# Kernel optimization log

Hardware: AMD Instinct MI355X
Metric: run time of the kernel (lower is better)

## Reference

```python
import jax, jax.numpy as jnp
import numpy as np

B, N, K, D = 2, 4096, 20, 128
PH = 8          # pos_mlp hidden dim
AH = 4 * D      # attn_mlp hidden dim (attn_mlp_hidden_mult=4)


def setup_inputs() -> dict:
    key = jax.random.key(0)
    ks = jax.random.split(key, 12)
    s = 0.02
    f32 = jnp.float32
    return {
        "x": jax.random.normal(ks[0], (B, N, 3), f32),
        "pos": jax.random.normal(ks[1], (B, N, 3), f32),
        # linear1/2/3 (torch Linear: y = x @ W.T + b)
        "W1": jax.random.normal(ks[2], (D, 3), f32) * s,  "b1": jnp.zeros((D,), f32),
        "W2": jax.random.normal(ks[3], (D, D), f32) * s,  "b2": jnp.zeros((D,), f32),
        "W3": jax.random.normal(ks[4], (D, D), f32) * s,  "b3": jnp.zeros((D,), f32),
        # PointTransformerLayer params
        "Wqkv": jax.random.normal(ks[5], (3 * D, D), f32) * s,          # to_qkv, no bias
        "Wp1": jax.random.normal(ks[6], (PH, 3), f32) * s,  "bp1": jnp.zeros((PH,), f32),
        "Wp2": jax.random.normal(ks[7], (D, PH), f32) * s,  "bp2": jnp.zeros((D,), f32),
        "Wa1": jax.random.normal(ks[8], (AH, D), f32) * s,  "ba1": jnp.zeros((AH,), f32),
        "Wa2": jax.random.normal(ks[9], (D, AH), f32) * s,  "ba2": jnp.zeros((D,), f32),
    }


def reference(x, pos, W1, b1, W2, b2, W3, b3, Wqkv,
              Wp1, bp1, Wp2, bp2, Wa1, ba1, Wa2, ba2):
    h = x @ W1.T + b1            # [B,N,D] linear1
    h1 = h @ W2.T + b2           # [B,N,D] linear2

    # --- PointTransformerLayer (lucidrains, KNN vector attention) ---
    qkv = h1 @ Wqkv.T            # [B,N,3D]
    q, k, v = jnp.split(qkv, 3, axis=-1)

    # squared pairwise distances and K nearest neighbors (self included)
    d2 = jnp.sum((pos[:, :, None, :] - pos[:, None, :, :]) ** 2, axis=-1)  # [B,N,N]
    _, idx = jax.lax.top_k(-d2, K)                                          # [B,N,K]

    gather = jax.vmap(lambda arr, ind: arr[ind])  # per-batch gather -> [B,N,K,*]
    kn = gather(k, idx)          # [B,N,K,D]
    vn = gather(v, idx)          # [B,N,K,D]
    pn = gather(pos, idx)        # [B,N,K,3]

    rel = pos[:, :, None, :] - pn                                   # [B,N,K,3]
    pe = jax.nn.relu(rel @ Wp1.T + bp1) @ Wp2.T + bp2               # pos_mlp [B,N,K,D]

    vn = vn + pe
    sim = jax.nn.relu((q[:, :, None, :] - kn + pe) @ Wa1.T + ba1) @ Wa2.T + ba2  # attn_mlp
    attn = jax.nn.softmax(sim, axis=2)                              # softmax over neighbors
    agg = jnp.sum(attn * vn, axis=2)                                # [B,N,D]

    return h + (agg @ W3.T + b3)  # residual: x + linear3(x1)
```

## Files before the change

### kernel.cpp

```cpp
#include <hip/hip_runtime.h>
#include <stdint.h>

#define BB 2
#define NN 4096
#define KNB 20
#define DD 128
#define PHH 8
#define AHH 512
#define BN (BB*NN)

typedef unsigned short ushort_t;
typedef short bf16x8 __attribute__((ext_vector_type(8)));
typedef float f32x4 __attribute__((ext_vector_type(4)));

__device__ __forceinline__ uint32_t umin32(uint32_t a, uint32_t b) { return a < b ? a : b; }
__device__ __forceinline__ uint32_t umax32(uint32_t a, uint32_t b) { return a > b ? a : b; }

__device__ __forceinline__ float bf2f(ushort_t u) {
    union { float f; uint32_t i; } c; c.i = ((uint32_t)u) << 16; return c.f;
}
__device__ __forceinline__ uint32_t cvt_pk_bf16(float lo, float hi) {
    uint32_t r;
    asm("v_cvt_pk_bf16_f32 %0, %1, %2" : "=v"(r) : "v"(lo), "v"(hi));
    return r;
}
__device__ __forceinline__ ushort_t f2bf(float f) {
    return (ushort_t)(cvt_pk_bf16(f, f) & 0xFFFFu);
}
__device__ __forceinline__ bf16x8 load_bfrag(const float* __restrict__ src) {
    float4 x = *(const float4*)src;
    float4 y = *(const float4*)(src + 4);
    union { bf16x8 v; uint32_t u[4]; } r;
    r.u[0] = cvt_pk_bf16(x.x, x.y);
    r.u[1] = cvt_pk_bf16(x.z, x.w);
    r.u[2] = cvt_pk_bf16(y.x, y.y);
    r.u[3] = cvt_pk_bf16(y.z, y.w);
    return r.v;
}

#define SW256(m, byteInRow) ((m)*256 + ((byteInRow) ^ (((m)&7) << 4)))

__global__ __launch_bounds__(256) void k_prep(
        const float* __restrict__ Wa1f, const float* __restrict__ Wa2f,
        const float* __restrict__ W3f, const float* __restrict__ W2f,
        const float* __restrict__ Wqkvf, const float* __restrict__ Wp2f,
        const float* __restrict__ pos,
        ushort_t* __restrict__ Wa1bf, ushort_t* __restrict__ Wa2bf,
        ushort_t* __restrict__ W3bf, ushort_t* __restrict__ W2bf,
        ushort_t* __restrict__ Wqkvbf, ushort_t* __restrict__ Wfusebf,
        float* __restrict__ psoa) {
    int bid = blockIdx.x, tid = threadIdx.x;
    if (bid < 64) {
        int base = bid * 2048 + tid * 8;
        const float* src = (base < 65536) ? (Wa1f + base) : (Wa2f + (base - 65536));
        ushort_t* dst = (base < 65536) ? (Wa1bf + base) : (Wa2bf + (base - 65536));
        union { ushort_t u[8]; uint4 q; } pk;
        #pragma unroll
        for (int i = 0; i < 8; ++i) pk.u[i] = f2bf(src[i]);
        *(uint4*)dst = pk.q;
    } else if (bid < 72) {
        int base = (bid - 64) * 2048 + tid * 8;
        union { ushort_t u[8]; uint4 q; } pk;
        #pragma unroll
        for (int i = 0; i < 8; ++i) pk.u[i] = f2bf(W3f[base + i]);
        *(uint4*)&W3bf[base] = pk.q;
    } else if (bid < 80) {
        int base = (bid - 72) * 2048 + tid * 8;
        union { ushort_t u[8]; uint4 q; } pk;
        #pragma unroll
        for (int i = 0; i < 8; ++i) pk.u[i] = f2bf(W2f[base + i]);
        *(uint4*)&W2bf[base] = pk.q;
    } else if (bid < 104) {
        int base = (bid - 80) * 2048 + tid * 8;
        union { ushort_t u[8]; uint4 q; } pk;
        #pragma unroll
        for (int i = 0; i < 8; ++i) pk.u[i] = f2bf(Wqkvf[base + i]);
        *(uint4*)&Wqkvbf[base] = pk.q;
    } else if (bid < 106) {
        int a = (bid - 104) * 256 + tid;
        float s[PHH];
        #pragma unroll
        for (int jj = 0; jj < PHH; ++jj) s[jj] = 0.f;
        for (int d = 0; d < DD; ++d) {
            float wv = Wa1f[(size_t)a*DD + d];
            #pragma unroll
            for (int jj = 0; jj < PHH; ++jj) s[jj] += wv * Wp2f[d*PHH + jj];
        }
        union { ushort_t u[8]; uint4 q; } pk;
        #pragma unroll
        for (int jj = 0; jj < PHH; ++jj) pk.u[jj] = f2bf(s[jj]);
        *(uint4*)&Wfusebf[a*PHH] = pk.q;
    } else {
        int e0 = (bid - 106) * 2048 + tid * 8;
        float v[8];
        #pragma unroll
        for (int i = 0; i < 8; ++i) {
            int el = e0 + i;
            int comp = el >> 13;
            int rem = el & 8191;
            v[i] = pos[(size_t)rem*3 + comp];
        }
        #pragma unroll
        for (int i = 0; i < 8; i += 4)
            *(float4*)&psoa[e0 + i] = (float4){v[i], v[i+1], v[i+2], v[i+3]};
    }
}

__global__ __launch_bounds__(256) void k_front(
        const float* __restrict__ x,
        const float* __restrict__ W1, const float* __restrict__ b1,
        const ushort_t* __restrict__ W2bf, const float* __restrict__ b2,
        const ushort_t* __restrict__ Wqkvbf,
        const ushort_t* __restrict__ Wa1bf, const float* __restrict__ ba1,
        float* __restrict__ h, ushort_t* __restrict__ vf,
        ushort_t* __restrict__ QWbf, ushort_t* __restrict__ KWbf) {
    __shared__ __align__(16) char smem[16896];
    float* xs = (float*)(smem + 16384);
    int tid = threadIdx.x, w = tid >> 6, lane = tid & 63;
    int lg = lane >> 4, c16 = lane & 15;
    int p0 = blockIdx.x * 32;

    if (tid < 96) xs[tid] = x[(size_t)p0*3 + tid];
    __syncthreads();

    #pragma unroll
    for (int it = 0; it < 16; ++it) {
        int lin = it*256 + tid;
        int m = lin >> 7, d = lin & 127;
        float hv = b1[d] + xs[m*3+0]*W1[d*3+0] + xs[m*3+1]*W1[d*3+1] + xs[m*3+2]*W1[d*3+2];
        h[(size_t)(p0+m)*DD + d] = hv;
        *(ushort_t*)&smem[SW256(m, d*2)] = f2bf(hv);
    }
    __syncthreads();

    {
        f32x4 acc[2][2];
        #pragma unroll
        for (int mt = 0; mt < 2; ++mt)
            #pragma unroll
            for (int ntl = 0; ntl < 2; ++ntl) acc[mt][ntl] = (f32x4){0,0,0,0};
        #pragma unroll
        for (int ks = 0; ks < 4; ++ks) {
            int k0 = ks*32 + lg*8;
            bf16x8 aF[2];
            #pragma unroll
            for (int mt = 0; mt < 2; ++mt)
                aF[mt] = *(const bf16x8*)&smem[SW256(mt*16 + c16, k0*2)];
            #pragma unroll
            for (int ntl = 0; ntl < 2; ++ntl) {
                int n = (2*w + ntl)*16 + c16;
                bf16x8 bF = *(const bf16x8*)&W2bf[(size_t)n*DD + k0];
                #pragma unroll
                for (int mt = 0; mt < 2; ++mt)
                    acc[mt][ntl] = __builtin_amdgcn_mfma_f32_16x16x32_bf16(aF[mt], bF, acc[mt][ntl], 0, 0, 0);
            }
        }
        #pragma unroll
        for (int ntl = 0; ntl < 2; ++ntl) {
            int n = (2*w + ntl)*16 + c16;
            float bias = b2[n];
            #pragma unroll
            for (int mt = 0; mt < 2; ++mt)
                #pragma unroll
                for (int i = 0; i < 4; ++i) {
                    int m = mt*16 + lg*4 + i;
                    *(ushort_t*)&smem[8192 + SW256(m, n*2)] = f2bf(acc[mt][ntl][i] + bias);
                }
        }
    }
    __syncthreads();

    {
        f32x4 acc[2][6];
        #pragma unroll
        for (int mt = 0; mt < 2; ++mt)
            #pragma unroll
            for (int ntl = 0; ntl < 6; ++ntl) acc[mt][ntl] = (f32x4){0,0,0,0};
        #pragma unroll
        for (int ks = 0; ks < 4; ++ks) {
            int k0 = ks*32 + lg*8;
            bf16x8 aF[2];
            #pragma unroll
            for (int mt = 0; mt < 2; ++mt)
                aF[mt] = *(const bf16x8*)&smem[8192 + SW256(mt*16 + c16, k0*2)];
            #pragma unroll
            for (int ntl = 0; ntl < 6; ++ntl) {
                int n = (w*6 + ntl)*16 + c16;
                bf16x8 bF = *(const bf16x8*)&Wqkvbf[(size_t)n*DD + k0];
                #pragma unroll
                for (int mt = 0; mt < 2; ++mt)
                    acc[mt][ntl] = __builtin_amdgcn_mfma_f32_16x16x32_bf16(aF[mt], bF, acc[mt][ntl], 0, 0, 0);
            }
        }
        #pragma unroll
        for (int ntl = 0; ntl < 6; ++ntl) {
            int n = (w*6 + ntl)*16 + c16;
            int r = n >> 7, d = n & 127;
            #pragma unroll
            for (int mt = 0; mt < 2; ++mt)
                #pragma unroll
                for (int i = 0; i < 4; ++i) {
                    int m = mt*16 + lg*4 + i;
                    if (r == 0) *(ushort_t*)&smem[SW256(m, d*2)] = f2bf(acc[mt][ntl][i]);
                    else if (r == 2) vf[(size_t)(p0+m)*DD + d] = f2bf(acc[mt][ntl][i]);
                }
        }
        __syncthreads();
        #pragma unroll
        for (int ntl = 0; ntl < 6; ++ntl) {
            int n = (w*6 + ntl)*16 + c16;
            int r = n >> 7, d = n & 127;
            if (r == 1) {
                #pragma unroll
                for (int mt = 0; mt < 2; ++mt)
                    #pragma unroll
                    for (int i = 0; i < 4; ++i) {
                        int m = mt*16 + lg*4 + i;
                        *(ushort_t*)&smem[8192 + SW256(m, d*2)] = f2bf(acc[mt][ntl][i]);
                    }
            }
        }
    }
    __syncthreads();

    #pragma unroll
    for (int half = 0; half < 2; ++half) {
        f32x4 accQ[2][4], accK[2][4];
        #pragma unroll
        for (int mt = 0; mt < 2; ++mt)
            #pragma unroll
            for (int ntl = 0; ntl < 4; ++ntl) {
                accQ[mt][ntl] = (f32x4){0,0,0,0};
                accK[mt][ntl] = (f32x4){0,0,0,0};
            }
        #pragma unroll
        for (int ks = 0; ks < 4; ++ks) {
            int k0 = ks*32 + lg*8;
            bf16x8 aQ[2], aK[2];
            #pragma unroll
            for (int mt = 0; mt < 2; ++mt) {
                aQ[mt] = *(const bf16x8*)&smem[SW256(mt*16 + c16, k0*2)];
                aK[mt] = *(const bf16x8*)&smem[8192 + SW256(mt*16 + c16, k0*2)];
            }
            #pragma unroll
            for (int ntl = 0; ntl < 4; ++ntl) {
                int n = (w*8 + half*4 + ntl)*16 + c16;
                bf16x8 bF = *(const bf16x8*)&Wa1bf[(size_t)n*DD + k0];
                #pragma unroll
                for (int mt = 0; mt < 2; ++mt) {
                    accQ[mt][ntl] = __builtin_amdgcn_mfma_f32_16x16x32_bf16(aQ[mt], bF, accQ[mt][ntl], 0, 0, 0);
                    accK[mt][ntl] = __builtin_amdgcn_mfma_f32_16x16x32_bf16(aK[mt], bF, accK[mt][ntl], 0, 0, 0);
                }
            }
        }
        #pragma unroll
        for (int ntl = 0; ntl < 4; ++ntl) {
            int n = (w*8 + half*4 + ntl)*16 + c16;
            float bias = ba1[n];
            #pragma unroll
            for (int mt = 0; mt < 2; ++mt)
                #pragma unroll
                for (int i = 0; i < 4; ++i) {
                    int m = mt*16 + lg*4 + i;
                    QWbf[(size_t)(p0+m)*AHH + n] = f2bf(accQ[mt][ntl][i] + bias);
                    KWbf[(size_t)(p0+m)*AHH + n] = f2bf(accK[mt][ntl][i]);
                }
        }
    }
}

__global__ __launch_bounds__(256) void k_knn(const float* __restrict__ pos,
                                             const float* __restrict__ psoa,
                                             int* __restrict__ idx) {
    int wid  = threadIdx.x >> 6;
    int lane = threadIdx.x & 63;
    int p = blockIdx.x*4 + wid;
    int b = p >> 12;
    float qx = pos[p*3+0], qy = pos[p*3+1], qz = pos[p*3+2];
    const float4* px4 = (const float4*)(psoa + (size_t)b*NN);
    const float4* py4 = (const float4*)(psoa + 8192 + (size_t)b*NN);
    const float4* pz4 = (const float4*)(psoa + 16384 + (size_t)b*NN);

    uint32_t bk[KNB];
    #pragma unroll
    for (int i = 0; i < KNB; ++i) bk[i] = 0xFFFFFFFFu;

    for (int it = 0; it < NN/256; ++it) {
        int j4 = it*64 + lane;
        float4 X = px4[j4], Y = py4[j4], Z = pz4[j4];
        #pragma unroll
        for (int c = 0; c < 4; ++c) {
            float dx = qx - ((c==0)?X.x:(c==1)?X.y:(c==2)?X.z:X.w);
            float dy = qy - ((c==0)?Y.x:(c==1)?Y.y:(c==2)?Y.z:Y.w);
            float dz = qz - ((c==0)?Z.x:(c==1)?Z.y:(c==2)?Z.z:Z.w);
            float d2 = dx*dx + dy*dy + dz*dz;
            uint32_t key = (__float_as_uint(d2) & 0xFFFFF000u) | (uint32_t)(j4*4 + c);
            if (key < bk[KNB-1]) {
                uint32_t cc = key;
                #pragma unroll
                for (int t = 0; t < KNB; ++t) {
                    uint32_t lo = umin32(cc, bk[t]);
                    uint32_t hi = umax32(cc, bk[t]);
                    bk[t] = lo; cc = hi;
                }
            }
        }
    }
    for (int r = 0; r < KNB; ++r) {
        uint32_t m = bk[0];
        #pragma unroll
        for (int s = 1; s < 64; s <<= 1)
            m = umin32(m, (uint32_t)__shfl_xor((int)m, s, 64));
        if (lane == 0) idx[(size_t)p*KNB + r] = (int)(m & 0xFFFu);
        bool win = (bk[0] == m);
        #pragma unroll
        for (int t = 0; t < KNB-1; ++t) bk[t] = win ? bk[t+1] : bk[t];
        bk[KNB-1] = win ? 0xFFFFFFFFu : bk[KNB-1];
    }
}

#define TL_OFF 0
#define PH_OFF 20480
#define NIDX_OFF 21760

__global__ __launch_bounds__(256, 4) void k_attn(
        const float* __restrict__ pos,
        const ushort_t* __restrict__ QWbf, const ushort_t* __restrict__ KWbf,
        const ushort_t* __restrict__ vf, const int* __restrict__ idx,
        const float* __restrict__ Wp1, const float* __restrict__ bp1,
        const float* __restrict__ Wp2, const float* __restrict__ bp2,
        const ushort_t* __restrict__ Wfusebf,
        const ushort_t* __restrict__ Wa2bf, const float* __restrict__ ba2,
        const ushort_t* __restrict__ W3bf, const float* __restrict__ b3,
        const float* __restrict__ h, float* __restrict__ out) {
    __shared__ __align__(16) char smem[22080];
    int* nidx = (int*)(smem + NIDX_OFF);

    int tid = threadIdx.x, w = tid >> 6, lane = tid & 63;
    int lg = lane >> 4, c16 = lane & 15;
    int bid = blockIdx.x;
    int xcd = bid & 7, sloc = bid >> 3;
    int b = xcd >> 2;
    int p0 = b*NN + ((xcd & 3)*256 + sloc)*4;

    if (tid < 80) nidx[tid] = idx[(size_t)(p0 + tid/20)*KNB + (tid%20)];
    __syncthreads();

    if (tid < 80) {
        int m = tid, g = m / 20;
        int j = nidx[m];
        const float* pq = pos + (size_t)(p0+g)*3;
        const float* pn = pos + (size_t)(b*NN+j)*3;
        float r0 = pq[0]-pn[0], r1 = pq[1]-pn[1], r2 = pq[2]-pn[2];
        union { ushort_t u[8]; uint4 q; } pk;
        #pragma unroll
        for (int jj = 0; jj < PHH; ++jj) {
            float a = bp1[jj] + r0*Wp1[jj*3+0] + r1*Wp1[jj*3+1] + r2*Wp1[jj*3+2];
            pk.u[jj] = f2bf(fmaxf(a, 0.f));
        }
        *(uint4*)&smem[PH_OFF + m*16] = pk.q;
    }
    __syncthreads();

    int dA = w*32 + 2*c16, dB = dA + 1;
    float bp2A = bp2[dA], bp2B = bp2[dB];
    float ba2A = ba2[dA], ba2B = ba2[dB];

    bf16x8 bP0 = {0,0,0,0,0,0,0,0}, bP1 = {0,0,0,0,0,0,0,0};
    if (lg == 0) {
        bP0 = load_bfrag(Wp2 + (size_t)dA*PHH);
        bP1 = load_bfrag(Wp2 + (size_t)dB*PHH);
    }
    uint32_t vpe_pk[5][4];
    #pragma unroll
    for (int mt = 0; mt < 5; ++mt) {
        bf16x8 aP = {0,0,0,0,0,0,0,0};
        if (lg == 0) aP = *(const bf16x8*)&smem[PH_OFF + (mt*16 + c16)*16];
        f32x4 accP0 = (f32x4){0,0,0,0}, accP1 = (f32x4){0,0,0,0};
        accP0 = __builtin_amdgcn_mfma_f32_16x16x32_bf16(aP, bP0, accP0, 0, 0, 0);
        accP1 = __builtin_amdgcn_mfma_f32_16x16x32_bf16(aP, bP1, accP1, 0, 0, 0);
        #pragma unroll
        for (int i = 0; i < 4; ++i) {
            int m = mt*16 + lg*4 + i;
            int j = nidx[m];
            uint32_t vw = *(const uint32_t*)&vf[(size_t)(b*NN+j)*DD + dA];
            float peA = accP0[i] + bp2A;
            float peB = accP1[i] + bp2B;
            vpe_pk[mt][i] = cvt_pk_bf16(bf2f((ushort_t)(vw & 0xFFFFu)) + peA,
                                        bf2f((ushort_t)(vw >> 16)) + peB);
        }
    }

    f32x4 accS[5][2];
    #pragma unroll
    for (int mt = 0; mt < 5; ++mt)
        #pragma unroll
        for (int ntl = 0; ntl < 2; ++ntl) accS[mt][ntl] = (f32x4){0,0,0,0};

    for (int c = 0; c < 4; ++c) {
        int aQ0 = c*128 + dA;
        bf16x8 bF0 = {0,0,0,0,0,0,0,0}, bF1 = {0,0,0,0,0,0,0,0};
        if (lg == 0) {
            bF0 = *(const bf16x8*)&Wfusebf[(size_t)aQ0*PHH];
            bF1 = *(const bf16x8*)&Wfusebf[(size_t)(aQ0+1)*PHH];
        }
        uint32_t qww[4];
        #pragma unroll
        for (int g = 0; g < 4; ++g)
            qww[g] = *(const uint32_t*)&QWbf[(size_t)(p0+g)*AHH + aQ0];
        uint32_t kwn[4];
        #pragma unroll
        for (int i = 0; i < 4; ++i)
            kwn[i] = *(const uint32_t*)&KWbf[(size_t)(b*NN + nidx[lg*4 + i])*AHH + aQ0];
        #pragma unroll
        for (int mt = 0; mt < 5; ++mt) {
            uint32_t kwc[4];
            #pragma unroll
            for (int i = 0; i < 4; ++i) kwc[i] = kwn[i];
            if (mt < 4) {
                #pragma unroll
                for (int i = 0; i < 4; ++i)
                    kwn[i] = *(const uint32_t*)&KWbf[(size_t)(b*NN + nidx[(mt+1)*16 + lg*4 + i])*AHH + aQ0];
            }
            bf16x8 aP = {0,0,0,0,0,0,0,0};
            if (lg == 0) aP = *(const bf16x8*)&smem[PH_OFF + (mt*16 + c16)*16];
            f32x4 accF0 = (f32x4){0,0,0,0}, accF1 = (f32x4){0,0,0,0};
            accF0 = __builtin_amdgcn_mfma_f32_16x16x32_bf16(aP, bF0, accF0, 0, 0, 0);
            accF1 = __builtin_amdgcn_mfma_f32_16x16x32_bf16(aP, bF1, accF1, 0, 0, 0);
            uint32_t qsel = (mt==0) ? qww[0]
                          : (mt==1) ? (lg>=1 ? qww[1] : qww[0])
                          : (mt==2) ? (lg>=2 ? qww[2] : qww[1])
                          : (mt==3) ? (lg==3 ? qww[3] : qww[2])
                          : qww[3];
            float qA = bf2f((ushort_t)(qsel & 0xFFFFu));
            float qB = bf2f((ushort_t)(qsel >> 16));
            #pragma unroll
            for (int i = 0; i < 4; ++i) {
                int m = mt*16 + lg*4 + i;
                float kA = bf2f((ushort_t)(kwc[i] & 0xFFFFu));
                float kB = bf2f((ushort_t)(kwc[i] >> 16));
                float tA = fmaxf(qA - kA + accF0[i], 0.f);
                float tB = fmaxf(qB - kB + accF1[i], 0.f);
                *(uint32_t*)&smem[TL_OFF + SW256(m, dA*2)] = cvt_pk_bf16(tA, tB);
            }
        }
        __syncthreads();

        __builtin_amdgcn_s_setprio(1);
        #pragma unroll
        for (int ks = 0; ks < 4; ++ks) {
            int k0 = ks*32 + lg*8;
            bf16x8 aF[5];
            #pragma unroll
            for (int mt = 0; mt < 5; ++mt)
                aF[mt] = *(const bf16x8*)&smem[TL_OFF + SW256(mt*16 + c16, k0*2)];
            bf16x8 bW0 = *(const bf16x8*)&Wa2bf[(size_t)dA*AHH + c*128 + k0];
            bf16x8 bW1 = *(const bf16x8*)&Wa2bf[(size_t)dB*AHH + c*128 + k0];
            #pragma unroll
            for (int mt = 0; mt < 5; ++mt) {
                accS[mt][0] = __builtin_amdgcn_mfma_f32_16x16x32_bf16(aF[mt], bW0, accS[mt][0], 0, 0, 0);
                accS[mt][1] = __builtin_amdgcn_mfma_f32_16x16x32_bf16(aF[mt], bW1, accS[mt][1], 0, 0, 0);
            }
        }
        __builtin_amdgcn_s_setprio(0);
        __syncthreads();
    }

    float s_mtA[5], a_mtA[5], s_mtB[5], a_mtB[5];
    #pragma unroll
    for (int mt = 0; mt < 5; ++mt) {
        float sa = 0.f, aa = 0.f, sb = 0.f, ab = 0.f;
        #pragma unroll
        for (int i = 0; i < 4; ++i) {
            float eA = __expf(accS[mt][0][i] + ba2A);
            float eB = __expf(accS[mt][1][i] + ba2B);
            uint32_t pk = vpe_pk[mt][i];
            float vA = bf2f((ushort_t)(pk & 0xFFFFu));
            float vB = bf2f((ushort_t)(pk >> 16));
            sa += eA; aa += eA*vA;
            sb += eB; ab += eB*vB;
        }
        s_mtA[mt] = sa; a_mtA[mt] = aa; s_mtB[mt] = sb; a_mtB[mt] = ab;
    }
    bool eq0 = (lg==0), ge1 = (lg>=1), ge2 = (lg>=2), le1 = (lg<=1), le2 = (lg<=2), eq3 = (lg==3);
    float s0A = s_mtA[0] + (eq0 ? s_mtA[1] : 0.f);
    float s1A = (ge1 ? s_mtA[1] : 0.f) + (le1 ? s_mtA[2] : 0.f);
    float s2A = (ge2 ? s_mtA[2] : 0.f) + (le2 ? s_mtA[3] : 0.f);
    float s3A = (eq3 ? s_mtA[3] : 0.f) + s_mtA[4];
    float a0A = a_mtA[0] + (eq0 ? a_mtA[1] : 0.f);
    float a1A = (ge1 ? a_mtA[1] : 0.f) + (le1 ? a_mtA[2] : 0.f);
    float a2A = (ge2 ? a_mtA[2] : 0.f) + (le2 ? a_mtA[3] : 0.f);
    float a3A = (eq3 ? a_mtA[3] : 0.f) + a_mtA[4];
    float s0B = s_mtB[0] + (eq0 ? s_mtB[1] : 0.f);
    float s1B = (ge1 ? s_mtB[1] : 0.f) + (le1 ? s_mtB[2] : 0.f);
    float s2B = (ge2 ? s_mtB[2] : 0.f) + (le2 ? s_mtB[3] : 0.f);
    float s3B = (eq3 ? s_mtB[3] : 0.f) + s_mtB[4];
    float a0B = a_mtB[0] + (eq0 ? a_mtB[1] : 0.f);
    float a1B = (ge1 ? a_mtB[1] : 0.f) + (le1 ? a_mtB[2] : 0.f);
    float a2B = (ge2 ? a_mtB[2] : 0.f) + (le2 ? a_mtB[3] : 0.f);
    float a3B = (eq3 ? a_mtB[3] : 0.f) + a_mtB[4];

    #define RED2(v) { v += __shfl_xor(v, 16, 64); v += __shfl_xor(v, 32, 64); }
    RED2(s0A) RED2(s1A) RED2(s2A) RED2(s3A)
    RED2(a0A) RED2(a1A) RED2(a2A) RED2(a3A)
    RED2(s0B) RED2(s1B) RED2(s2B) RED2(s3B)
    RED2(a0B) RED2(a1B) RED2(a2B) RED2(a3B)
    #undef RED2

    float myS_A = (lg==0) ? s0A : (lg==1) ? s1A : (lg==2) ? s2A : s3A;
    float myA_A = (lg==0) ? a0A : (lg==1) ? a1A : (lg==2) ? a2A : a3A;
    float myS_B = (lg==0) ? s0B : (lg==1) ? s1B : (lg==2) ? s2B : s3B;
    float myA_B = (lg==0) ? a0B : (lg==1) ? a1B : (lg==2) ? a2B : a3B;
    float aggA = myA_A / myS_A;
    float aggB = myA_B / myS_B;

    float hv[2][4];
    if (lg == 0) {
        #pragma unroll
        for (int ntl = 0; ntl < 2; ++ntl) {
            int n = (w*2 + ntl)*16 + c16;
            #pragma unroll
            for (int i = 0; i < 4; ++i)
                hv[ntl][i] = h[(size_t)(p0+i)*DD + n];
        }
    }
    #pragma unroll
    for (int z = 0; z < 3; ++z)
        *(uint32_t*)&smem[TL_OFF + 1024 + (z*256 + tid)*4] = 0u;
    *(uint32_t*)&smem[TL_OFF + SW256(lg, dA*2)] = cvt_pk_bf16(aggA, aggB);
    __syncthreads();

    f32x4 accO[2];
    accO[0] = (f32x4){0,0,0,0}; accO[1] = (f32x4){0,0,0,0};
    #pragma unroll
    for (int ks = 0; ks < 4; ++ks) {
        int k0 = ks*32 + lg*8;
        bf16x8 aF = *(const bf16x8*)&smem[TL_OFF + SW256(c16, k0*2)];
        #pragma unroll
        for (int ntl = 0; ntl < 2; ++ntl) {
            int n = (w*2 + ntl)*16 + c16;
            bf16x8 bF = *(const bf16x8*)&W3bf[(size_t)n*DD + k0];
            accO[ntl] = __builtin_amdgcn_mfma_f32_16x16x32_bf16(aF, bF, accO[ntl], 0, 0, 0);
        }
    }
    if (lg == 0) {
        #pragma unroll
        for (int ntl = 0; ntl < 2; ++ntl) {
            int n = (w*2 + ntl)*16 + c16;
            float bias = b3[n];
            #pragma unroll
            for (int i = 0; i < 4; ++i) {
                size_t o = (size_t)(p0+i)*DD + n;
                out[o] = accO[ntl][i] + bias + hv[ntl][i];
            }
        }
    }
}

extern "C" void kernel_launch(void* const* d_in, const int* in_sizes, int n_in,
                              void* d_out, int out_size, void* d_ws, size_t ws_size,
                              hipStream_t stream) {
    const float* x    = (const float*)d_in[0];
    const float* pos  = (const float*)d_in[1];
    const float* W1   = (const float*)d_in[2];
    const float* b1   = (const float*)d_in[3];
    const float* W2   = (const float*)d_in[4];
    const float* b2   = (const float*)d_in[5];
    const float* W3   = (const float*)d_in[6];
    const float* b3   = (const float*)d_in[7];
    const float* Wqkv = (const float*)d_in[8];
    const float* Wp1  = (const float*)d_in[9];
    const float* bp1  = (const float*)d_in[10];
    const float* Wp2  = (const float*)d_in[11];
    const float* bp2  = (const float*)d_in[12];
    const float* Wa1  = (const float*)d_in[13];
    const float* ba1  = (const float*)d_in[14];
    const float* Wa2  = (const float*)d_in[15];
    const float* ba2  = (const float*)d_in[16];

    char* W = (char*)d_ws;
    float*    h       = (float*)(W + 0);
    ushort_t* vf      = (ushort_t*)(W + 8388608);
    ushort_t* QWbf    = (ushort_t*)(W + 10485760);
    ushort_t* KWbf    = (ushort_t*)(W + 18874368);
    int*      idx     = (int*)(W + 27262976);
    ushort_t* Wa1bf   = (ushort_t*)(W + 27918336);
    ushort_t* Wa2bf   = (ushort_t*)(W + 28049408);
    ushort_t* Wfusebf = (ushort_t*)(W + 28180480);
    float*    psoa    = (float*)(W + 28188672);
    ushort_t* W3bf    = (ushort_t*)(W + 28286976);
    ushort_t* W2bf    = (ushort_t*)(W + 28319744);
    ushort_t* Wqkvbf  = (ushort_t*)(W + 28352512);

    k_prep <<<118, 256, 0, stream>>>(Wa1, Wa2, W3, W2, Wqkv, Wp2, pos,
                                     Wa1bf, Wa2bf, W3bf, W2bf, Wqkvbf, Wfusebf, psoa);
    k_front<<<BN/32, 256, 0, stream>>>(x, W1, b1, W2bf, b2, Wqkvbf, Wa1bf, ba1,
                                       h, vf, QWbf, KWbf);
    k_knn  <<<BN/4, 256, 0, stream>>>(pos, psoa, idx);
    k_attn <<<BN/4, 256, 0, stream>>>(pos, QWbf, KWbf, vf, idx,
                                      Wp1, bp1, Wp2, bp2, Wfusebf, Wa2bf, ba2,
                                      W3bf, b3, h, (float*)d_out);
}
```

Before: 159.0 us.

## Order attention query points by Morton cell to improve neighbor-gather locality

Adds two extra blocks to the front kernel that bucket each batch's points into a 16^3 Morton-coded grid, using a counting sort with shared-memory atomics, and write a permutation. The attention kernel then processes query points in this spatially sorted order, so blocks that run near each other gather overlapping KNN neighbor rows of KW and v, which is meant to raise L2/cache hit rates. The cost is an extra indirection per query and scattered writes to the output, and the order within a cell is nondeterministic because of the atomics.

```diff
diff --git a/kernel.cpp b/kernel.cpp
--- a/kernel.cpp
+++ b/kernel.cpp
@@ -36,6 +36,15 @@
     r.u[2] = cvt_pk_bf16(y.x, y.y);
     r.u[3] = cvt_pk_bf16(y.z, y.w);
     return r.v;
+}
+__device__ __forceinline__ uint32_t exp3b(uint32_t v) {
+    return (v & 1u) | ((v & 2u) << 2) | ((v & 4u) << 4) | ((v & 8u) << 6);
+}
+__device__ __forceinline__ uint32_t mcell(float x, float y, float z) {
+    uint32_t ux = (uint32_t)fminf(fmaxf((x + 4.f) * 2.f, 0.f), 15.f);
+    uint32_t uy = (uint32_t)fminf(fmaxf((y + 4.f) * 2.f, 0.f), 15.f);
+    uint32_t uz = (uint32_t)fminf(fmaxf((z + 4.f) * 2.f, 0.f), 15.f);
+    return (exp3b(ux) << 2) | (exp3b(uy) << 1) | exp3b(uz);
 }
 
 #define SW256(m, byteInRow) ((m)*256 + ((byteInRow) ^ (((m)&7) << 4)))
@@ -107,18 +116,57 @@
 }
 
 __global__ __launch_bounds__(256) void k_front(
-        const float* __restrict__ x,
+        const float* __restrict__ x, const float* __restrict__ posg,
         const float* __restrict__ W1, const float* __restrict__ b1,
         const ushort_t* __restrict__ W2bf, const float* __restrict__ b2,
         const ushort_t* __restrict__ Wqkvbf,
         const ushort_t* __restrict__ Wa1bf, const float* __restrict__ ba1,
         float* __restrict__ h, ushort_t* __restrict__ vf,
-        ushort_t* __restrict__ QWbf, ushort_t* __restrict__ KWbf) {
-    __shared__ __align__(16) char smem[16896];
+        ushort_t* __restrict__ QWbf, ushort_t* __restrict__ KWbf,
+        int* __restrict__ perm) {
+    __shared__ __align__(16) char smem[17408];
+    int tid = threadIdx.x, bid = blockIdx.x;
+
+    if (bid >= BN/32) {
+        int bb = bid - BN/32;
+        uint32_t* cnt  = (uint32_t*)smem;
+        uint32_t* part = (uint32_t*)(smem + 16384);
+        const float* pb = posg + (size_t)bb*NN*3;
+        for (int i = tid; i < 4096; i += 256) cnt[i] = 0;
+        __syncthreads();
+        for (int i = tid; i < NN; i += 256) {
+            uint32_t c = mcell(pb[i*3+0], pb[i*3+1], pb[i*3+2]);
+            atomicAdd(&cnt[c], 1u);
+        }
+        __syncthreads();
+        uint32_t s = 0;
+        #pragma unroll
+        for (int j = 0; j < 16; ++j) s += cnt[tid*16 + j];
+        part[tid] = s;
+        __syncthreads();
+        if (tid == 0) {
+            uint32_t run = 0;
+            for (int i = 0; i < 256; ++i) { uint32_t c = part[i]; part[i] = run; run += c; }
+        }
+        __syncthreads();
+        {
+            uint32_t run = part[tid];
+            #pragma unroll
+            for (int j = 0; j < 16; ++j) { uint32_t c = cnt[tid*16 + j]; cnt[tid*16 + j] = run; run += c; }
+        }
+        __syncthreads();
+        for (int i = tid; i < NN; i += 256) {
+            uint32_t c = mcell(pb[i*3+0], pb[i*3+1], pb[i*3+2]);
+            uint32_t posn = atomicAdd(&cnt[c], 1u);
+            perm[(size_t)bb*NN + posn] = bb*NN + i;
+        }
+        return;
+    }
+
     float* xs = (float*)(smem + 16384);
-    int tid = threadIdx.x, w = tid >> 6, lane = tid & 63;
+    int w = tid >> 6, lane = tid & 63;
     int lg = lane >> 4, c16 = lane & 15;
-    int p0 = blockIdx.x * 32;
+    int p0 = bid * 32;
 
     if (tid < 96) xs[tid] = x[(size_t)p0*3 + tid];
     __syncthreads();
@@ -322,34 +370,39 @@
 #define TL_OFF 0
 #define PH_OFF 20480
 #define NIDX_OFF 21760
+#define QP_OFF 22080
 
 __global__ __launch_bounds__(256, 4) void k_attn(
         const float* __restrict__ pos,
         const ushort_t* __restrict__ QWbf, const ushort_t* __restrict__ KWbf,
         const ushort_t* __restrict__ vf, const int* __restrict__ idx,
+        const int* __restrict__ perm,
         const float* __restrict__ Wp1, const float* __restrict__ bp1,
         const float* __restrict__ Wp2, const float* __restrict__ bp2,
         const ushort_t* __restrict__ Wfusebf,
         const ushort_t* __restrict__ Wa2bf, const float* __restrict__ ba2,
         const ushort_t* __restrict__ W3bf, const float* __restrict__ b3,
         const float* __restrict__ h, float* __restrict__ out) {
-    __shared__ __align__(16) char smem[22080];
+    __shared__ __align__(16) char smem[22096];
     int* nidx = (int*)(smem + NIDX_OFF);
+    int* qpS  = (int*)(smem + QP_OFF);
 
     int tid = threadIdx.x, w = tid >> 6, lane = tid & 63;
     int lg = lane >> 4, c16 = lane & 15;
     int bid = blockIdx.x;
     int xcd = bid & 7, sloc = bid >> 3;
     int b = xcd >> 2;
-    int p0 = b*NN + ((xcd & 3)*256 + sloc)*4;
-
-    if (tid < 80) nidx[tid] = idx[(size_t)(p0 + tid/20)*KNB + (tid%20)];
+    int slot4 = ((xcd & 3)*256 + sloc)*4;
+
+    if (tid < 4) qpS[tid] = perm[(size_t)b*NN + slot4 + tid];
+    __syncthreads();
+    if (tid < 80) nidx[tid] = idx[(size_t)qpS[tid/20]*KNB + (tid%20)];
     __syncthreads();
 
     if (tid < 80) {
         int m = tid, g = m / 20;
         int j = nidx[m];
-        const float* pq = pos + (size_t)(p0+g)*3;
+        const float* pq = pos + (size_t)qpS[g]*3;
         const float* pn = pos + (size_t)(b*NN+j)*3;
         float r0 = pq[0]-pn[0], r1 = pq[1]-pn[1], r2 = pq[2]-pn[2];
         union { ushort_t u[8]; uint4 q; } pk;
@@ -407,7 +460,7 @@
         uint32_t qww[4];
         #pragma unroll
         for (int g = 0; g < 4; ++g)
-            qww[g] = *(const uint32_t*)&QWbf[(size_t)(p0+g)*AHH + aQ0];
+            qww[g] = *(const uint32_t*)&QWbf[(size_t)qpS[g]*AHH + aQ0];
         uint32_t kwn[4];
         #pragma unroll
         for (int i = 0; i < 4; ++i)
@@ -521,7 +574,7 @@
             int n = (w*2 + ntl)*16 + c16;
             #pragma unroll
             for (int i = 0; i < 4; ++i)
-                hv[ntl][i] = h[(size_t)(p0+i)*DD + n];
+                hv[ntl][i] = h[(size_t)qpS[i]*DD + n];
         }
     }
     #pragma unroll
@@ -550,7 +603,7 @@
             float bias = b3[n];
             #pragma unroll
             for (int i = 0; i < 4; ++i) {
-                size_t o = (size_t)(p0+i)*DD + n;
+                size_t o = (size_t)qpS[i]*DD + n;
                 out[o] = accO[ntl][i] + bias + hv[ntl][i];
             }
         }
@@ -591,13 +644,14 @@
     ushort_t* W3bf    = (ushort_t*)(W + 28286976);
     ushort_t* W2bf    = (ushort_t*)(W + 28319744);
     ushort_t* Wqkvbf  = (ushort_t*)(W + 28352512);
+    int*      perm    = (int*)(W + 28450816);
 
     k_prep <<<118, 256, 0, stream>>>(Wa1, Wa2, W3, W2, Wqkv, Wp2, pos,
                                      Wa1bf, Wa2bf, W3bf, W2bf, Wqkvbf, Wfusebf, psoa);
-    k_front<<<BN/32, 256, 0, stream>>>(x, W1, b1, W2bf, b2, Wqkvbf, Wa1bf, ba1,
-                                       h, vf, QWbf, KWbf);
+    k_front<<<BN/32 + 2, 256, 0, stream>>>(x, pos, W1, b1, W2bf, b2, Wqkvbf, Wa1bf, ba1,
+                                           h, vf, QWbf, KWbf, perm);
     k_knn  <<<BN/4, 256, 0, stream>>>(pos, psoa, idx);
-    k_attn <<<BN/4, 256, 0, stream>>>(pos, QWbf, KWbf, vf, idx,
+    k_attn <<<BN/4, 256, 0, stream>>>(pos, QWbf, KWbf, vf, idx, perm,
                                       Wp1, bp1, Wp2, bp2, Wfusebf, Wa2bf, ba2,
                                       W3bf, b3, h, (float*)d_out);
 }
```

After: 159.6 us (median of 2 runs). About the same (+0.3%).
